# Kernel tuning notes

Hardware: AMD Instinct MI355X
Metric: run time of the kernel (lower is better)

## Reference

```python
import jax, jax.numpy as jnp
import numpy as np

B, N, F = 1024, 784, 1
C1, C2, H, NCLS = 32, 32, 512, 10


def setup_inputs() -> dict:
    key = jax.random.key(0)
    ks = jax.random.split(key, 10)
    x = jax.random.normal(ks[0], (B, N, F), jnp.float32)
    # dense (renormalized-style) adjacency, shared across the batch; rows roughly sum to ~1
    a = jax.random.uniform(ks[1], (N, N), jnp.float32) * (2.0 / N)
    def glorot(k, shape):
        lim = np.sqrt(6.0 / (shape[0] + shape[1])).astype(np.float32)
        return jax.random.uniform(k, shape, jnp.float32, -lim, lim)
    return {
        "x": x,
        "a": a,
        "w1": glorot(ks[2], (F, C1)),
        "b1": jnp.zeros((C1,), jnp.float32),
        "w2": glorot(ks[3], (C1, C2)),
        "b2": jnp.zeros((C2,), jnp.float32),
        "wf1": glorot(ks[4], (N * C2, H)),
        "bf1": jnp.zeros((H,), jnp.float32),
        "wf2": glorot(ks[5], (H, NCLS)),
        "bf2": jnp.zeros((NCLS,), jnp.float32),
    }


def _graph_conv(x, a, w, b):
    # Spektral GraphConv (batch mode): elu(A @ (X @ W) + b)
    xw = jnp.einsum('bnf,fc->bnc', x, w)
    agg = jnp.einsum('nm,bmc->bnc', a, xw)
    return jax.nn.elu(agg + b)


def reference(x, a, w1, b1, w2, b2, wf1, bf1, wf2, bf2):
    h = _graph_conv(x, a, w1, b1)          # [B, N, 32]
    h = _graph_conv(h, a, w2, b2)          # [B, N, 32]
    h = h.reshape(h.shape[0], -1)          # Flatten -> [B, N*32]
    h = jax.nn.relu(h @ wf1 + bf1)         # [B, 512]
    return jax.nn.softmax(h @ wf2 + bf2, axis=-1)  # [B, 10]
```

## Files before the change

kernel.cpp:

```cpp
#include <hip/hip_runtime.h>
#include <hip/hip_bf16.h>
#include <math.h>

#define BATCH 1024
#define NREAL 784
#define NPAD  896
#define C1D   32
#define C2D   32
#define HDIM  512
#define NCLS  10
#define KFC   25088

#define KS_G1 4
#define KS_FC 16

#define BM 128
#define BN 128
#define BK 32

using bf16x8  = __attribute__((ext_vector_type(8))) __bf16;
using floatx4 = __attribute__((ext_vector_type(4))) float;

__device__ __forceinline__ void gll16(const void* g, void* l) {
    __builtin_amdgcn_global_load_lds((const __attribute__((address_space(1))) void*)g,
                                     (__attribute__((address_space(3))) void*)l,
                                     16, 0, 0);
}

__device__ __forceinline__ float elu_f(float t) {
    return t > 0.f ? t : (__expf(t) - 1.f);
}

template<int MODE>
__launch_bounds__(256)
__global__ void gemm_bt(const __hip_bfloat16* __restrict__ A, int lda,
                        const __hip_bfloat16* __restrict__ Bm, int ldb,
                        int kIters, int kPerZ, size_t sliceStride,
                        float* __restrict__ outF, int ldc,
                        __hip_bfloat16* __restrict__ outH,
                        const float* __restrict__ bias)
{
    __shared__ __align__(16) __hip_bfloat16 As[2][BM * BK];
    __shared__ __align__(16) __hip_bfloat16 Bs[2][BN * BK];

    const int tid  = threadIdx.x;
    const int lane = tid & 63;
    const int wave = tid >> 6;
    const int wi = wave >> 1, wj = wave & 1;

    const int m0 = blockIdx.y * BM;
    const int n0 = blockIdx.x * BN;
    const int kBase = blockIdx.z * kPerZ;

    const int rowInChunk = lane >> 2;
    const int kOff8 = (lane & 3) * 8;

    const __hip_bfloat16* aSrc[2];
    const __hip_bfloat16* bSrc[2];
    #pragma unroll
    for (int c = 0; c < 2; c++) {
        const int r = (wave * 2 + c) * 16 + rowInChunk;
        aSrc[c] = A  + (size_t)(m0 + r) * lda + kBase + kOff8;
        bSrc[c] = Bm + (size_t)(n0 + r) * ldb + kBase + kOff8;
    }

    floatx4 acc[4][4];
    const floatx4 zero4 = {0.f, 0.f, 0.f, 0.f};
    #pragma unroll
    for (int i = 0; i < 4; i++)
        #pragma unroll
        for (int j = 0; j < 4; j++) acc[i][j] = zero4;

    #pragma unroll
    for (int c = 0; c < 2; c++) {
        const int chunk = wave * 2 + c;
        gll16(aSrc[c], &As[0][chunk * 512]);
        gll16(bSrc[c], &Bs[0][chunk * 512]);
        aSrc[c] += BK; bSrc[c] += BK;
    }

    for (int kt = 0; kt < kIters; ++kt) {
        const int buf = kt & 1;
        __syncthreads();

        if (kt + 1 < kIters) {
            const int nbuf = buf ^ 1;
            #pragma unroll
            for (int c = 0; c < 2; c++) {
                const int chunk = wave * 2 + c;
                gll16(aSrc[c], &As[nbuf][chunk * 512]);
                gll16(bSrc[c], &Bs[nbuf][chunk * 512]);
                aSrc[c] += BK; bSrc[c] += BK;
            }
        }

        bf16x8 af[4], bfr[4];
        #pragma unroll
        for (int mi = 0; mi < 4; mi++)
            af[mi] = *(const bf16x8*)(&As[buf][(wi * 64 + mi * 16 + (lane & 15)) * BK + (lane >> 4) * 8]);
        #pragma unroll
        for (int nj = 0; nj < 4; nj++)
            bfr[nj] = *(const bf16x8*)(&Bs[buf][(wj * 64 + nj * 16 + (lane & 15)) * BK + (lane >> 4) * 8]);

        #pragma unroll
        for (int mi = 0; mi < 4; mi++)
            #pragma unroll
            for (int nj = 0; nj < 4; nj++)
                acc[mi][nj] = __builtin_amdgcn_mfma_f32_16x16x32_bf16(af[mi], bfr[nj], acc[mi][nj], 0, 0, 0);
    }

    #pragma unroll
    for (int mi = 0; mi < 4; mi++) {
        #pragma unroll
        for (int nj = 0; nj < 4; nj++) {
            #pragma unroll
            for (int r = 0; r < 4; r++) {
                const int row = m0 + wi * 64 + mi * 16 + (lane >> 4) * 4 + r;
                const int col = n0 + wj * 64 + nj * 16 + (lane & 15);
                const float v = acc[mi][nj][r];
                if (MODE == 1) {
                    if (row < NREAL) {
                        const int c = col & 31, b = col >> 5;
                        const float t = elu_f(v + bias[c]);
                        outH[(size_t)b * KFC + row * 32 + c] = __float2bfloat16(t);
                    }
                } else {
                    outF[(size_t)blockIdx.z * sliceStride + (size_t)row * ldc + col] = v;
                }
            }
        }
    }
}

__global__ void convX(const float* __restrict__ x, __hip_bfloat16* __restrict__ Xbf) {
    const int idx = blockIdx.x * 256 + threadIdx.x;
    if (idx >= BATCH * NPAD) return;
    const int m = idx % NPAD, b = idx / NPAD;
    const float v = (m < NREAL) ? x[(size_t)b * NREAL + m] : 0.f;
    Xbf[idx] = __float2bfloat16(v);
}

__global__ void convA(const float* __restrict__ a, __hip_bfloat16* __restrict__ Abf) {
    const int idx = blockIdx.x * 256 + threadIdx.x;
    if (idx >= NPAD * NPAD) return;
    const int m = idx % NPAD, n = idx / NPAD;
    const float v = (m < NREAL && n < NREAL) ? a[(size_t)n * NREAL + m] : 0.f;
    Abf[idx] = __float2bfloat16(v);
}

__global__ void convW(const float* __restrict__ wf1, __hip_bfloat16* __restrict__ Wt) {
    __shared__ float tile[32][33];
    const int k0 = blockIdx.x * 32, h0 = blockIdx.y * 32;
    const int tx = threadIdx.x, ty = threadIdx.y;
    #pragma unroll
    for (int i = 0; i < 4; i++)
        tile[ty * 4 + i][tx] = wf1[(size_t)(k0 + ty * 4 + i) * HDIM + h0 + tx];
    __syncthreads();
    #pragma unroll
    for (int i = 0; i < 4; i++)
        Wt[(size_t)(h0 + ty * 4 + i) * KFC + k0 + tx] = __float2bfloat16(tile[tx][ty * 4 + i]);
}

__global__ void layer1_fuse(const float* __restrict__ Ypart,
                            const float* __restrict__ w1, const float* __restrict__ b1,
                            const float* __restrict__ w2,
                            __hip_bfloat16* __restrict__ Tt)
{
    __shared__ __align__(16) float sW2[C1D * C2D];
    __shared__ float sw1[C1D], sb1[C1D];
    const int tid = threadIdx.x;
    for (int i = tid; i < C1D * C2D; i += 128) sW2[i] = w2[i];
    if (tid < C1D) { sw1[tid] = w1[tid]; sb1[tid] = b1[tid]; }
    __syncthreads();

    const int m = blockIdx.x * 128 + tid;
    const int b = blockIdx.y;
    float y = 0.f;
    #pragma unroll
    for (int z = 0; z < KS_G1; z++)
        y += Ypart[(size_t)z * (BATCH * NPAD) + (size_t)b * NPAD + m];

    float h[C1D];
    #pragma unroll
    for (int c1 = 0; c1 < C1D; c1++) h[c1] = elu_f(y * sw1[c1] + sb1[c1]);

    float4 t4[8];
    #pragma unroll
    for (int q = 0; q < 8; q++) t4[q] = make_float4(0.f, 0.f, 0.f, 0.f);
    #pragma unroll
    for (int c1 = 0; c1 < C1D; c1++) {
        const float hv = h[c1];
        const float4* row = (const float4*)(sW2 + c1 * C2D);
        #pragma unroll
        for (int q = 0; q < 8; q++) {
            const float4 w = row[q];
            t4[q].x += hv * w.x; t4[q].y += hv * w.y;
            t4[q].z += hv * w.z; t4[q].w += hv * w.w;
        }
    }
    const float* tf = (const float*)t4;
    #pragma unroll
    for (int c = 0; c < C2D; c++)
        Tt[((size_t)(b * 32 + c)) * NPAD + m] = __float2bfloat16(tf[c]);
}

__global__ void reduceFc1(const float* __restrict__ part, const float* __restrict__ bf1,
                          float* __restrict__ h3)
{
    const int idx = blockIdx.x * 256 + threadIdx.x;
    if (idx >= BATCH * HDIM) return;
    float s = 0.f;
    #pragma unroll
    for (int z = 0; z < KS_FC; z++) s += part[(size_t)z * (BATCH * HDIM) + idx];
    s += bf1[idx & (HDIM - 1)];
    h3[idx] = s > 0.f ? s : 0.f;
}

__global__ void fc2_softmax(const float* __restrict__ h3, const float* __restrict__ wf2,
                            const float* __restrict__ bf2, float* __restrict__ out)
{
    __shared__ float sW[HDIM * NCLS];
    __shared__ float sb[NCLS];
    const int tid = threadIdx.x;
    for (int i = tid; i < HDIM * NCLS; i += 256) sW[i] = wf2[i];
    if (tid < NCLS) sb[tid] = bf2[tid];
    __syncthreads();

    const int lane = tid & 63, wave = tid >> 6;
    const int b = blockIdx.x * 4 + wave;

    float acc[NCLS];
    #pragma unroll
    for (int c = 0; c < NCLS; c++) acc[c] = 0.f;
    #pragma unroll
    for (int q = 0; q < 8; q++) {
        const int h = q * 64 + lane;
        const float hv = h3[(size_t)b * HDIM + h];
        #pragma unroll
        for (int c = 0; c < NCLS; c++) acc[c] += hv * sW[h * NCLS + c];
    }
    #pragma unroll
    for (int c = 0; c < NCLS; c++) {
        #pragma unroll
        for (int off = 32; off >= 1; off >>= 1) acc[c] += __shfl_down(acc[c], off);
    }
    if (lane == 0) {
        float mx = -1e30f;
        #pragma unroll
        for (int c = 0; c < NCLS; c++) { acc[c] += sb[c]; mx = fmaxf(mx, acc[c]); }
        float e[NCLS], s = 0.f;
        #pragma unroll
        for (int c = 0; c < NCLS; c++) { e[c] = __expf(acc[c] - mx); s += e[c]; }
        const float inv = 1.f / s;
        #pragma unroll
        for (int c = 0; c < NCLS; c++) out[(size_t)b * NCLS + c] = e[c] * inv;
    }
}

extern "C" void kernel_launch(void* const* d_in, const int* in_sizes, int n_in,
                              void* d_out, int out_size, void* d_ws, size_t ws_size,
                              hipStream_t stream)
{
    const float* x   = (const float*)d_in[0];
    const float* a   = (const float*)d_in[1];
    const float* w1  = (const float*)d_in[2];
    const float* b1  = (const float*)d_in[3];
    const float* w2  = (const float*)d_in[4];
    const float* b2  = (const float*)d_in[5];
    const float* wf1 = (const float*)d_in[6];
    const float* bf1 = (const float*)d_in[7];
    const float* wf2 = (const float*)d_in[8];
    const float* bf2 = (const float*)d_in[9];
    float* out = (float*)d_out;

    char* ws = (char*)d_ws;
    __hip_bfloat16* h2f  = (__hip_bfloat16*)(ws + 0);
    float*          Ypart= (float*)(ws + 0);
    __hip_bfloat16* Tt   = (__hip_bfloat16*)(ws + 51380224);
    __hip_bfloat16* Wt   = (__hip_bfloat16*)(ws + 51380224);
    float*          part = (float*)(ws + 77070336);
    __hip_bfloat16* Abf  = (__hip_bfloat16*)(ws + 110100480);
    __hip_bfloat16* Xbf  = (__hip_bfloat16*)(ws + 111706112);
    float*          h3   = (float*)(ws + 113541120);

    convX<<<(BATCH * NPAD + 255) / 256, 256, 0, stream>>>(x, Xbf);
    convA<<<(NPAD * NPAD + 255) / 256, 256, 0, stream>>>(a, Abf);

    gemm_bt<2><<<dim3(NPAD / BN, BATCH / BM, KS_G1), 256, 0, stream>>>(
        Xbf, NPAD, Abf, NPAD, (NPAD / KS_G1) / BK, NPAD / KS_G1,
        (size_t)BATCH * NPAD, Ypart, NPAD, nullptr, nullptr);

    layer1_fuse<<<dim3(NPAD / 128, BATCH), 128, 0, stream>>>(Ypart, w1, b1, w2, Tt);

    gemm_bt<1><<<dim3((BATCH * 32) / BN, NPAD / BM, 1), 256, 0, stream>>>(
        Abf, NPAD, Tt, NPAD, NPAD / BK, 0, 0, nullptr, 0, h2f, b2);

    convW<<<dim3(KFC / 32, HDIM / 32), dim3(32, 8), 0, stream>>>(wf1, Wt);

    gemm_bt<2><<<dim3(HDIM / BN, BATCH / BM, KS_FC), 256, 0, stream>>>(
        h2f, KFC, Wt, KFC, (KFC / KS_FC) / BK, KFC / KS_FC,
        (size_t)BATCH * HDIM, part, HDIM, nullptr, nullptr);

    reduceFc1<<<(BATCH * HDIM + 255) / 256, 256, 0, stream>>>(part, bf1, h3);

    fc2_softmax<<<BATCH / 4, 256, 0, stream>>>(h3, wf2, bf2, out);
}
```

Measured before the change: 306.3 us.

## Replace direct-to-LDS loads with register-staged prefetch and fuse fc1 reduction into softmax

The GEMM main loop no longer uses global_load_lds. It prefetches tiles two K-steps ahead into registers, writes the next tile into the alternate LDS buffer while computing the current one, and synchronises with a custom waitcnt+barrier. Separately, the split-K reduction plus bias and ReLU for fc1 moves into the fc2/softmax kernel, which drops one launch and the h3 round trip through global memory. The register staging costs more VGPRs and extra LDS writes, and may lower occupancy. The fused softmax kernel now reads all 16 partial slices itself, with less parallelism than the old reduction kernel.

New measurement: 608.0 us. 98.5% more time.

```diff
diff --git a/kernel.cpp b/kernel.cpp
--- a/kernel.cpp
+++ b/kernel.cpp
@@ -21,14 +21,12 @@
 using bf16x8  = __attribute__((ext_vector_type(8))) __bf16;
 using floatx4 = __attribute__((ext_vector_type(4))) float;
 
-__device__ __forceinline__ void gll16(const void* g, void* l) {
-    __builtin_amdgcn_global_load_lds((const __attribute__((address_space(1))) void*)g,
-                                     (__attribute__((address_space(3))) void*)l,
-                                     16, 0, 0);
-}
-
 __device__ __forceinline__ float elu_f(float t) {
     return t > 0.f ? t : (__expf(t) - 1.f);
+}
+
+__device__ __forceinline__ void wg_barrier_lds() {
+    asm volatile("s_waitcnt lgkmcnt(0)\n\ts_barrier" ::: "memory");
 }
 
 template<int MODE>
@@ -63,6 +61,8 @@
         aSrc[c] = A  + (size_t)(m0 + r) * lda + kBase + kOff8;
         bSrc[c] = Bm + (size_t)(n0 + r) * ldb + kBase + kOff8;
     }
+    const int ldsW[2] = { (wave * 2 + 0) * 512 + lane * 8,
+                          (wave * 2 + 1) * 512 + lane * 8 };
 
     floatx4 acc[4][4];
     const floatx4 zero4 = {0.f, 0.f, 0.f, 0.f};
@@ -71,42 +71,68 @@
         #pragma unroll
         for (int j = 0; j < 4; j++) acc[i][j] = zero4;
 
+    int4 sa[2][2], sb[2][2];
+
     #pragma unroll
     for (int c = 0; c < 2; c++) {
-        const int chunk = wave * 2 + c;
-        gll16(aSrc[c], &As[0][chunk * 512]);
-        gll16(bSrc[c], &Bs[0][chunk * 512]);
+        sa[0][c] = *(const int4*)aSrc[c];
+        sb[0][c] = *(const int4*)bSrc[c];
         aSrc[c] += BK; bSrc[c] += BK;
     }
-
-    for (int kt = 0; kt < kIters; ++kt) {
-        const int buf = kt & 1;
-        __syncthreads();
-
-        if (kt + 1 < kIters) {
-            const int nbuf = buf ^ 1;
+    if (kIters > 1) {
+        #pragma unroll
+        for (int c = 0; c < 2; c++) {
+            sa[1][c] = *(const int4*)aSrc[c];
+            sb[1][c] = *(const int4*)bSrc[c];
+            aSrc[c] += BK; bSrc[c] += BK;
+        }
+    }
+    #pragma unroll
+    for (int c = 0; c < 2; c++) {
+        *(int4*)(&As[0][ldsW[c]]) = sa[0][c];
+        *(int4*)(&Bs[0][ldsW[c]]) = sb[0][c];
+    }
+    wg_barrier_lds();
+
+    for (int kt = 0; kt < kIters; kt += 2) {
+        #pragma unroll
+        for (int u = 0; u < 2; u++) {
+            const int k = kt + u;
+            if (k >= kIters) break;
+            const int buf = u;
+
+            bf16x8 af[4], bfr[4];
             #pragma unroll
-            for (int c = 0; c < 2; c++) {
-                const int chunk = wave * 2 + c;
-                gll16(aSrc[c], &As[nbuf][chunk * 512]);
-                gll16(bSrc[c], &Bs[nbuf][chunk * 512]);
-                aSrc[c] += BK; bSrc[c] += BK;
-            }
-        }
-
-        bf16x8 af[4], bfr[4];
-        #pragma unroll
-        for (int mi = 0; mi < 4; mi++)
-            af[mi] = *(const bf16x8*)(&As[buf][(wi * 64 + mi * 16 + (lane & 15)) * BK + (lane >> 4) * 8]);
-        #pragma unroll
-        for (int nj = 0; nj < 4; nj++)
-            bfr[nj] = *(const bf16x8*)(&Bs[buf][(wj * 64 + nj * 16 + (lane & 15)) * BK + (lane >> 4) * 8]);
-
-        #pragma unroll
-        for (int mi = 0; mi < 4; mi++)
+            for (int mi = 0; mi < 4; mi++)
+                af[mi] = *(const bf16x8*)(&As[buf][(wi * 64 + mi * 16 + (lane & 15)) * BK + (lane >> 4) * 8]);
             #pragma unroll
             for (int nj = 0; nj < 4; nj++)
-                acc[mi][nj] = __builtin_amdgcn_mfma_f32_16x16x32_bf16(af[mi], bfr[nj], acc[mi][nj], 0, 0, 0);
+                bfr[nj] = *(const bf16x8*)(&Bs[buf][(wj * 64 + nj * 16 + (lane & 15)) * BK + (lane >> 4) * 8]);
+
+            if (k + 2 < kIters) {
+                #pragma unroll
+                for (int c = 0; c < 2; c++) {
+                    sa[u][c] = *(const int4*)aSrc[c];
+                    sb[u][c] = *(const int4*)bSrc[c];
+                    aSrc[c] += BK; bSrc[c] += BK;
+                }
+            }
+            if (k + 1 < kIters) {
+                #pragma unroll
+                for (int c = 0; c < 2; c++) {
+                    *(int4*)(&As[buf ^ 1][ldsW[c]]) = sa[u ^ 1][c];
+                    *(int4*)(&Bs[buf ^ 1][ldsW[c]]) = sb[u ^ 1][c];
+                }
+            }
+
+            #pragma unroll
+            for (int mi = 0; mi < 4; mi++)
+                #pragma unroll
+                for (int nj = 0; nj < 4; nj++)
+                    acc[mi][nj] = __builtin_amdgcn_mfma_f32_16x16x32_bf16(af[mi], bfr[nj], acc[mi][nj], 0, 0, 0);
+
+            wg_barrier_lds();
+        }
     }
 
     #pragma unroll
@@ -204,20 +230,9 @@
         Tt[((size_t)(b * 32 + c)) * NPAD + m] = __float2bfloat16(tf[c]);
 }
 
-__global__ void reduceFc1(const float* __restrict__ part, const float* __restrict__ bf1,
-                          float* __restrict__ h3)
-{
-    const int idx = blockIdx.x * 256 + threadIdx.x;
-    if (idx >= BATCH * HDIM) return;
-    float s = 0.f;
-    #pragma unroll
-    for (int z = 0; z < KS_FC; z++) s += part[(size_t)z * (BATCH * HDIM) + idx];
-    s += bf1[idx & (HDIM - 1)];
-    h3[idx] = s > 0.f ? s : 0.f;
-}
-
-__global__ void fc2_softmax(const float* __restrict__ h3, const float* __restrict__ wf2,
-                            const float* __restrict__ bf2, float* __restrict__ out)
+__global__ void fc2_softmax(const float* __restrict__ part, const float* __restrict__ bf1,
+                            const float* __restrict__ wf2, const float* __restrict__ bf2,
+                            float* __restrict__ out)
 {
     __shared__ float sW[HDIM * NCLS];
     __shared__ float sb[NCLS];
@@ -235,7 +250,11 @@
     #pragma unroll
     for (int q = 0; q < 8; q++) {
         const int h = q * 64 + lane;
-        const float hv = h3[(size_t)b * HDIM + h];
+        float hv = bf1[h];
+        #pragma unroll
+        for (int z = 0; z < KS_FC; z++)
+            hv += part[(size_t)z * (BATCH * HDIM) + (size_t)b * HDIM + h];
+        hv = hv > 0.f ? hv : 0.f;
         #pragma unroll
         for (int c = 0; c < NCLS; c++) acc[c] += hv * sW[h * NCLS + c];
     }
@@ -281,7 +300,6 @@
     float*          part = (float*)(ws + 77070336);
     __hip_bfloat16* Abf  = (__hip_bfloat16*)(ws + 110100480);
     __hip_bfloat16* Xbf  = (__hip_bfloat16*)(ws + 111706112);
-    float*          h3   = (float*)(ws + 113541120);
 
     convX<<<(BATCH * NPAD + 255) / 256, 256, 0, stream>>>(x, Xbf);
     convA<<<(NPAD * NPAD + 255) / 256, 256, 0, stream>>>(a, Abf);
@@ -301,7 +319,5 @@
         h2f, KFC, Wt, KFC, (KFC / KS_FC) / BK, KFC / KS_FC,
         (size_t)BATCH * HDIM, part, HDIM, nullptr, nullptr);
 
-    reduceFc1<<<(BATCH * HDIM + 255) / 256, 256, 0, stream>>>(part, bf1, h3);
-
-    fc2_softmax<<<BATCH / 4, 256, 0, stream>>>(h3, wf2, bf2, out);
-}
+    fc2_softmax<<<BATCH / 4, 256, 0, stream>>>(part, bf1, wf2, bf2, out);
+}
```
